# Performance work log

Hardware: AMD Instinct MI355X
Metric: run time of the kernel (lower is better)

## Reference

```python
import jax, jax.numpy as jnp
import numpy as np

N = 50000; E = 800000; F_IN = 128; H = 16; G = 256
DIMS = [F_IN, H, 2 * H, 4 * H, 4 * H, 8 * H]
EPS = 1e-5


def setup_inputs() -> dict:
    key = jax.random.key(0)
    ks = iter(jax.random.split(key, 40))
    inp = {}
    inp["x"] = jax.random.normal(next(ks), (N, F_IN), dtype=jnp.float32)
    inp["edge_index"] = jax.random.randint(next(ks), (2, E), 0, N, dtype=jnp.int32)
    inp["edge_weight"] = jax.random.uniform(next(ks), (E,), dtype=jnp.float32)
    inp["batch"] = jnp.sort(jax.random.randint(next(ks), (N,), 0, G, dtype=jnp.int32))
    for i in range(5):
        din, dout = DIMS[i], DIMS[i + 1]
        inp[f"W{i+1}"] = jax.random.normal(next(ks), (din, dout), dtype=jnp.float32) / np.sqrt(din).astype(np.float32)
        inp[f"b{i+1}"] = jnp.zeros((dout,), jnp.float32)
        inp[f"g{i+1}"] = jnp.ones((dout,), jnp.float32)
        inp[f"bt{i+1}"] = jnp.zeros((dout,), jnp.float32)
    inp["fc1_w"] = jax.random.normal(next(ks), (8 * H, 4 * H), dtype=jnp.float32) / np.sqrt(8 * H).astype(np.float32)
    inp["fc1_b"] = jnp.zeros((4 * H,), jnp.float32)
    inp["fc2_w"] = jax.random.normal(next(ks), (4 * H, 1), dtype=jnp.float32) / np.sqrt(4 * H).astype(np.float32)
    inp["fc2_b"] = jnp.zeros((1,), jnp.float32)
    return inp


def _gcn_norm(edge_index, edge_weight, n):
    # PyG GCNConv: add self-loops (weight 1), symmetric deg^-1/2 normalization.
    loop = jnp.arange(n, dtype=edge_index.dtype)
    row = jnp.concatenate([edge_index[0], loop])  # source
    col = jnp.concatenate([edge_index[1], loop])  # target
    w = jnp.concatenate([edge_weight, jnp.ones((n,), edge_weight.dtype)])
    deg = jax.ops.segment_sum(w, col, num_segments=n)
    dis = jnp.where(deg > 0, jax.lax.rsqrt(jnp.maximum(deg, 1e-12)), 0.0)
    return row, col, dis[row] * w * dis[col]


def _bn(h, g, b):
    # BatchNorm1d, training-mode batch statistics (biased variance, eps=1e-5)
    mu = h.mean(0)
    v = h.var(0)
    return g * (h - mu) * jax.lax.rsqrt(v + EPS) + b


def reference(x, edge_index, edge_weight, batch,
              W1, b1, g1, bt1, W2, b2, g2, bt2, W3, b3, g3, bt3,
              W4, b4, g4, bt4, W5, b5, g5, bt5,
              fc1_w, fc1_b, fc2_w, fc2_b):
    n = x.shape[0]
    row, col, norm = _gcn_norm(edge_index, edge_weight, n)

    def conv(h, W, b):
        m = h @ W                                   # [N, dout] dense transform
        agg = jax.ops.segment_sum(m[row] * norm[:, None], col, num_segments=n)
        return agg + b

    h = _bn(jax.nn.relu(conv(x, W1, b1)), g1, bt1)
    h = _bn(jax.nn.relu(conv(h, W2, b2)), g2, bt2)
    h = _bn(jax.nn.relu(conv(h, W3, b3)), g3, bt3)
    h = jax.nn.relu(_bn(conv(h, W4, b4), g4, bt4))   # layer4: conv->bn->relu
    h = _bn(conv(h, W5, b5), g5, bt5)                # layer5: conv->bn
    pooled = jax.ops.segment_sum(h, batch, num_segments=G)  # global_add_pool -> [G, 8H]
    p = jax.nn.relu(pooled)
    p = jax.nn.relu(p @ fc1_w + fc1_b)
    # dropout is identity in eval mode
    return (p @ fc2_w + fc2_b).reshape(-1)          # [G]
```

## Files before the change

### kernel.cpp

```cpp
#include <hip/hip_runtime.h>
#include <hip/hip_fp16.h>
#include <stdint.h>

#define NN 50000
#define NE 800000
#define NG 256
#define NBUCKET 16
#define PARTSZ (NBUCKET * 256)

#define NBKT 391
#define ABLK 391
#define ASLICE 2048
#define BCAP 2560

__device__ __forceinline__ float bf2f(unsigned short u) {
    return __uint_as_float(((unsigned)u) << 16);
}
__device__ __forceinline__ unsigned short f2bf(float f) {
    unsigned b = __float_as_uint(f);
    return (unsigned short)((b + 0x7FFF + ((b >> 16) & 1)) >> 16);
}
__device__ __forceinline__ unsigned short f2h(float f) {
    __half h = __float2half(f);
    return *(unsigned short*)&h;
}
__device__ __forceinline__ float h2f(unsigned short u) {
    __half h = *(__half*)&u;
    return __half2float(h);
}

#define AFF4(u, sc, sh) { u.x = fmaxf(sc.x*u.x+sh.x,0.f); u.y = fmaxf(sc.y*u.y+sh.y,0.f); \
                          u.z = fmaxf(sc.z*u.z+sh.z,0.f); u.w = fmaxf(sc.w*u.w+sh.w,0.f); }

__device__ __forceinline__ void scan_totals(const int* __restrict__ totals,
                                            int* __restrict__ sbase, int tid) {
    if (tid < 64) {
        const int C = (NBKT + 63) / 64;
        int tv[C];
        int s = 0;
        int i0 = tid * C;
#pragma unroll
        for (int j = 0; j < C; ++j) {
            int idx = i0 + j;
            int x = (idx < NBKT) ? totals[idx] : 0;
            tv[j] = x; s += x;
        }
        int inc = s;
        for (int off = 1; off < 64; off <<= 1) {
            int t2 = __shfl_up(inc, off, 64);
            if (tid >= off) inc += t2;
        }
        int run = inc - s;
#pragma unroll
        for (int j = 0; j < C; ++j) {
            int idx = i0 + j;
            if (idx < NBKT) sbase[idx] = run;
            run += tv[j];
        }
        if (tid == 63) sbase[NBKT] = run;
    }
}

__global__ void kA1(const int* __restrict__ col, int* __restrict__ bb, float* part, int e) {
    __shared__ int cnt[NBKT];
    for (int j = threadIdx.x; j < NBKT; j += 256) cnt[j] = 0;
    for (int i = blockIdx.x * 256 + threadIdx.x; i < 5 * PARTSZ; i += ABLK * 256) part[i] = 0.f;
    __syncthreads();
    int start = blockIdx.x * ASLICE;
    int end = min(start + ASLICE, e);
    for (int i = start + threadIdx.x; i < end; i += 256)
        atomicAdd(&cnt[col[i] >> 7], 1);
    __syncthreads();
    for (int j = threadIdx.x; j < NBKT; j += 256) bb[blockIdx.x * NBKT + j] = cnt[j];
}

__global__ void kA2a(int* __restrict__ bb, int* __restrict__ totals) {
    __shared__ int v[ABLK];
    int k = blockIdx.x;
    int tid = threadIdx.x;
    for (int b = tid; b < ABLK; b += 256) v[b] = bb[b * NBKT + k];
    __syncthreads();
    if (tid < 64) {
        const int C = (ABLK + 63) / 64;
        int tv[C];
        int s = 0;
        int i0 = tid * C;
#pragma unroll
        for (int j = 0; j < C; ++j) {
            int idx = i0 + j;
            int x = (idx < ABLK) ? v[idx] : 0;
            tv[j] = x; s += x;
        }
        int inc = s;
        for (int off = 1; off < 64; off <<= 1) {
            int t2 = __shfl_up(inc, off, 64);
            if (tid >= off) inc += t2;
        }
        int run = inc - s;
#pragma unroll
        for (int j = 0; j < C; ++j) {
            int idx = i0 + j;
            if (idx < ABLK) v[idx] = run;
            run += tv[j];
        }
        if (tid == 63) totals[k] = run;
    }
    __syncthreads();
    for (int b = tid; b < ABLK; b += 256) bb[b * NBKT + k] = v[b];
}

__global__ void kA3g(const int* __restrict__ row, const int* __restrict__ col,
                     const float* __restrict__ ew, const int* __restrict__ bb,
                     const int* __restrict__ totals, int2* __restrict__ staging,
                     const float* __restrict__ x, const float* __restrict__ W0,
                     float* __restrict__ m1, int e, int n) {
    __shared__ int cur[NBKT];
    __shared__ int sbase[NBKT + 1];
    __shared__ float Wl[128 * 16];
    int tid = threadIdx.x;
    if ((int)blockIdx.x < ABLK) {
        scan_totals(totals, sbase, tid);
        __syncthreads();
        for (int j = tid; j < NBKT; j += 256)
            cur[j] = sbase[j] + bb[blockIdx.x * NBKT + j];
        __syncthreads();
        int start = blockIdx.x * ASLICE;
        int end = min(start + ASLICE, e);
        for (int i = start + tid; i < end; i += 256) {
            int c = col[i];
            int p = atomicAdd(&cur[c >> 7], 1);
            staging[p] = make_int2(row[i] | ((c & 127) << 16), __float_as_int(ew[i]));
        }
        return;
    }
    int bid = (int)blockIdx.x - ABLK;
    for (int i = tid; i < 128 * 16 / 4; i += 256)
        ((float4*)Wl)[i] = ((const float4*)W0)[i];
    __syncthreads();
    int jq = tid % 4, group = tid / 4;
    int node0 = (bid * 64 + group) * 2;
    const float4* h4 = (const float4*)x;
    int hb[2]; bool val[2];
#pragma unroll
    for (int i = 0; i < 2; ++i) {
        int nd = node0 + i;
        val[i] = nd < n;
        hb[i] = (val[i] ? nd : n - 1) * 32;
    }
    float4 acc[2];
    acc[0] = {0,0,0,0}; acc[1] = {0,0,0,0};
#pragma unroll 4
    for (int k4 = 0; k4 < 32; ++k4) {
        const float* wb = &Wl[(k4 * 4) * 16 + jq * 4];
        float4 w0 = *(const float4*)(wb);
        float4 w1 = *(const float4*)(wb + 16);
        float4 w2 = *(const float4*)(wb + 32);
        float4 w3 = *(const float4*)(wb + 48);
#pragma unroll
        for (int i = 0; i < 2; ++i) {
            float4 hv = h4[hb[i] + k4];
            acc[i].x += hv.x*w0.x + hv.y*w1.x + hv.z*w2.x + hv.w*w3.x;
            acc[i].y += hv.x*w0.y + hv.y*w1.y + hv.z*w2.y + hv.w*w3.y;
            acc[i].z += hv.x*w0.z + hv.y*w1.z + hv.z*w2.z + hv.w*w3.z;
            acc[i].w += hv.x*w0.w + hv.y*w1.w + hv.z*w2.w + hv.w*w3.w;
        }
    }
#pragma unroll
    for (int i = 0; i < 2; ++i)
        if (val[i]) ((float4*)m1)[(node0 + i) * 4 + jq] = acc[i];
}

__global__ void __launch_bounds__(256) kB(const int* __restrict__ totals,
                                          const int2* __restrict__ staging,
                                          unsigned int* __restrict__ csr, int* __restrict__ ptr,
                                          float* __restrict__ dis, int n) {
    __shared__ int2 st[BCAP];
    __shared__ unsigned int outb[BCAP];
    __shared__ int hist[129];
    __shared__ int cur[128];
    __shared__ int sbase[NBKT + 1];
    int k = blockIdx.x, t = threadIdx.x;
    scan_totals(totals, sbase, t);
    if (t < 129) hist[t] = 0;
    __syncthreads();
    int base = sbase[k], cnt = sbase[k + 1] - sbase[k];
    int node0 = k << 7;
    int ncov = min(128, n - node0);
    if (cnt <= BCAP) {
        for (int i = t; i < cnt; i += 256) {
            int2 v = staging[base + i];
            st[i] = v;
            atomicAdd(&hist[v.x >> 16], 1);
        }
        __syncthreads();
        if (t == 0) {
            int run = 0;
            for (int j = 0; j < 128; ++j) { int h = hist[j]; hist[j] = run; run += h; }
            hist[128] = run;
        }
        __syncthreads();
        if (t < 128) cur[t] = hist[t];
        if (t < ncov) ptr[node0 + t] = base + hist[t];
        __syncthreads();
        for (int i = t; i < cnt; i += 256) {
            int2 v = st[i];
            int j = v.x >> 16;
            int p = atomicAdd(&cur[j], 1);
            outb[p] = (unsigned)(v.x & 0xFFFF) | ((unsigned)f2h(__int_as_float(v.y)) << 16);
        }
        __syncthreads();
        for (int i = t; i < cnt; i += 256) csr[base + i] = outb[i];
        if (t < ncov) {
            float s = 1.f;
            int a = hist[t], b2 = hist[t + 1];
            for (int p = a; p < b2; ++p) s += h2f((unsigned short)(outb[p] >> 16));
            dis[node0 + t] = rsqrtf(s);
        }
    } else {
        for (int i = t; i < cnt; i += 256) atomicAdd(&hist[staging[base + i].x >> 16], 1);
        __syncthreads();
        if (t == 0) {
            int run = 0;
            for (int j = 0; j < 128; ++j) { int h = hist[j]; hist[j] = run; run += h; }
            hist[128] = run;
        }
        __syncthreads();
        if (t < 128) cur[t] = hist[t];
        if (t < ncov) ptr[node0 + t] = base + hist[t];
        __syncthreads();
        for (int i = t; i < cnt; i += 256) {
            int2 v = staging[base + i];
            int j = v.x >> 16;
            int p = atomicAdd(&cur[j], 1);
            csr[base + p] = (unsigned)(v.x & 0xFFFF) | ((unsigned)f2h(__int_as_float(v.y)) << 16);
        }
        __threadfence_block();
        __syncthreads();
        if (t < ncov) {
            float s = 1.f;
            int a = hist[t], b2 = hist[t + 1];
            for (int p = a; p < b2; ++p) s += h2f((unsigned short)(csr[base + p] >> 16));
            dis[node0 + t] = rsqrtf(s);
        }
    }
    if (k == gridDim.x - 1 && t == 0) ptr[n] = sbase[NBKT];
}

__global__ void k_l1gather(const float* __restrict__ src, const int* __restrict__ ptr,
                           unsigned int* __restrict__ csr, const float* __restrict__ dis,
                           const float* __restrict__ bias, float* __restrict__ partOut,
                           float* __restrict__ out, int n) {
    __shared__ float ls[16], lq[16];
    int tid = threadIdx.x;
    if (tid < 16) { ls[tid] = 0.f; lq[tid] = 0.f; }
    __syncthreads();
    int t = blockIdx.x * 256 + tid;
    int node = t >> 2;
    int l4 = t & 3;
    bool valid = node < n;
    int nc = valid ? node : n - 1;
    const float4* s4 = (const float4*)src;
    float dc = dis[nc];
    float w0 = dc * dc;
    float4 v = s4[nc * 4 + l4];
    float4 acc = { w0 * v.x, w0 * v.y, w0 * v.z, w0 * v.w };
    int p0 = ptr[nc], p1 = ptr[nc + 1];
    int p = p0;
    for (; p + 4 <= p1; p += 4) {
        unsigned int c0 = csr[p], c1 = csr[p+1], c2 = csr[p+2], c3 = csr[p+3];
        int s0i = c0 & 0xFFFF, s1i = c1 & 0xFFFF, s2i = c2 & 0xFFFF, s3i = c3 & 0xFFFF;
        float e0 = dis[s0i] * h2f((unsigned short)(c0 >> 16)) * dc;
        float e1 = dis[s1i] * h2f((unsigned short)(c1 >> 16)) * dc;
        float e2 = dis[s2i] * h2f((unsigned short)(c2 >> 16)) * dc;
        float e3 = dis[s3i] * h2f((unsigned short)(c3 >> 16)) * dc;
        float4 u0 = s4[s0i * 4 + l4];
        float4 u1 = s4[s1i * 4 + l4];
        float4 u2 = s4[s2i * 4 + l4];
        float4 u3 = s4[s3i * 4 + l4];
        acc.x += e0*u0.x + e1*u1.x + e2*u2.x + e3*u3.x;
        acc.y += e0*u0.y + e1*u1.y + e2*u2.y + e3*u3.y;
        acc.z += e0*u0.z + e1*u1.z + e2*u2.z + e3*u3.z;
        acc.w += e0*u0.w + e1*u1.w + e2*u2.w + e3*u3.w;
        if (l4 == 0) {
            csr[p]   = (unsigned)s0i | ((unsigned)f2h(e0) << 16);
            csr[p+1] = (unsigned)s1i | ((unsigned)f2h(e1) << 16);
            csr[p+2] = (unsigned)s2i | ((unsigned)f2h(e2) << 16);
            csr[p+3] = (unsigned)s3i | ((unsigned)f2h(e3) << 16);
        }
    }
    for (; p < p1; ++p) {
        unsigned int ce = csr[p];
        int si = ce & 0xFFFF;
        float w = dis[si] * h2f((unsigned short)(ce >> 16)) * dc;
        float4 u = s4[si * 4 + l4];
        acc.x += w*u.x; acc.y += w*u.y; acc.z += w*u.z; acc.w += w*u.w;
        if (l4 == 0) csr[p] = (unsigned)si | ((unsigned)f2h(w) << 16);
    }
    float4 b = ((const float4*)bias)[l4];
    acc.x = fmaxf(acc.x + b.x, 0.f);
    acc.y = fmaxf(acc.y + b.y, 0.f);
    acc.z = fmaxf(acc.z + b.z, 0.f);
    acc.w = fmaxf(acc.w + b.w, 0.f);
    if (valid) ((float4*)out)[nc * 4 + l4] = acc;
    float s0 = valid ? acc.x : 0.f, s1 = valid ? acc.y : 0.f;
    float s2 = valid ? acc.z : 0.f, s3 = valid ? acc.w : 0.f;
    float q0 = s0*s0, q1 = s1*s1, q2 = s2*s2, q3 = s3*s3;
    for (int off = 4; off < 64; off <<= 1) {
        s0 += __shfl_down(s0, off, 64); s1 += __shfl_down(s1, off, 64);
        s2 += __shfl_down(s2, off, 64); s3 += __shfl_down(s3, off, 64);
        q0 += __shfl_down(q0, off, 64); q1 += __shfl_down(q1, off, 64);
        q2 += __shfl_down(q2, off, 64); q3 += __shfl_down(q3, off, 64);
    }
    int lane = tid & 63;
    if (lane < 4) {
        atomicAdd(&ls[4*lane+0], s0); atomicAdd(&ls[4*lane+1], s1);
        atomicAdd(&ls[4*lane+2], s2); atomicAdd(&ls[4*lane+3], s3);
        atomicAdd(&lq[4*lane+0], q0); atomicAdd(&lq[4*lane+1], q1);
        atomicAdd(&lq[4*lane+2], q2); atomicAdd(&lq[4*lane+3], q3);
    }
    __syncthreads();
    int bkt = (blockIdx.x & (NBUCKET - 1)) * 256;
    if (tid < 16) {
        atomicAdd(&partOut[bkt + tid], ls[tid]);
        atomicAdd(&partOut[bkt + 128 + tid], lq[tid]);
    }
}

template <int D, int BF16>
__device__ __forceinline__ float4 load_row(const void* src, int node, int l4) {
    if (BF16) {
        const unsigned short* sb = (const unsigned short*)src;
        ushort4 r = *(const ushort4*)(sb + (size_t)node * D + (l4 << 2));
        float4 f;
        f.x = bf2f(r.x); f.y = bf2f(r.y); f.z = bf2f(r.z); f.w = bf2f(r.w);
        return f;
    } else {
        const float4* s4 = (const float4*)src;
        return s4[(size_t)node * (D / 4) + l4];
    }
}

template <int D>
__device__ __forceinline__ void ldrow16(const unsigned short* __restrict__ src, int node, int l8,
                                        float4& a, float4& b) {
    uint4 r = *(const uint4*)(src + (size_t)node * D + (l8 << 3));
    a.x = bf2f((unsigned short)(r.x)); a.y = bf2f((unsigned short)(r.x >> 16));
    a.z = bf2f((unsigned short)(r.y)); a.w = bf2f((unsigned short)(r.y >> 16));
    b.x = bf2f((unsigned short)(r.z)); b.y = bf2f((unsigned short)(r.z >> 16));
    b.z = bf2f((unsigned short)(r.w)); b.w = bf2f((unsigned short)(r.w >> 16));
}

template <int DIN, int DOUT, int EP, int POSTAFF, int PREAFF, int RELU,
          int BF16IN, int BF16OUT, int NPB>
__global__ void __launch_bounds__(256) k_fused(
        const void* __restrict__ src, const int* __restrict__ ptr,
        const unsigned int* __restrict__ csr, const float* __restrict__ dis,
        const float* __restrict__ partIn, const float* __restrict__ gmv,
        const float* __restrict__ btv, const float* __restrict__ W,
        const float* __restrict__ bias, float* __restrict__ partOut,
        void* __restrict__ out, int n) {
    const int TPN1 = DIN / 4, LPN = TPN1 * EP, GN1 = 256 / LPN;
    const int TPN2 = DOUT / 4, G2 = 256 / TPN2;
    const int HS = DIN + 4;
    __shared__ float Wl[DIN * DOUT];
    __shared__ float hrow[NPB * HS];
    __shared__ float scs[DIN], shs[DIN];
    __shared__ float ls[DOUT], lq[DOUT];
    int tid = threadIdx.x;
    for (int i = tid; i < DIN * DOUT / 4; i += 256)
        ((float4*)Wl)[i] = ((const float4*)W)[i];
    if (tid < DIN) {
        float s = 0.f, q = 0.f;
#pragma unroll
        for (int b2 = 0; b2 < NBUCKET; ++b2) {
            s += partIn[b2 * 256 + tid];
            q += partIn[b2 * 256 + 128 + tid];
        }
        float mu = s / (float)n;
        float var = q / (float)n - mu * mu;
        float a = gmv[tid] * rsqrtf(var + 1e-5f);
        scs[tid] = a;
        shs[tid] = btv[tid] - mu * a;
    }
    if (tid < DOUT) { ls[tid] = 0.f; lq[tid] = 0.f; }
    __syncthreads();

    int nodebase = blockIdx.x * NPB;
    {
        int grp = tid / LPN, r = tid % LPN;
        int e0 = r / TPN1, l4 = r % TPN1;
        float4 sc = ((const float4*)scs)[l4];
        float4 sh = ((const float4*)shs)[l4];
#pragma unroll
        for (int pass = 0; pass < NPB / GN1; ++pass) {
            int nl = pass * GN1 + grp;
            int node = nodebase + nl;
            int nc = node < n ? node : n - 1;
            float4 acc = {0.f, 0.f, 0.f, 0.f};
            float sumw = 0.f;
            if (e0 == 0) {
                float d = dis[nc];
                float w0 = d * d;
                float4 v = load_row<DIN, BF16IN>(src, nc, l4);
                if (PREAFF) AFF4(v, sc, sh);
                acc.x = w0*v.x; acc.y = w0*v.y; acc.z = w0*v.z; acc.w = w0*v.w;
                sumw = w0;
            }
            int p0 = ptr[nc], p1 = ptr[nc + 1];
            int p = p0 + e0;
            for (; p + 3 * EP < p1; p += 4 * EP) {
                unsigned int c0 = csr[p], c1 = csr[p + EP], c2 = csr[p + 2*EP], c3 = csr[p + 3*EP];
                float e0w = h2f((unsigned short)(c0 >> 16)), e1w = h2f((unsigned short)(c1 >> 16));
                float e2w = h2f((unsigned short)(c2 >> 16)), e3w = h2f((unsigned short)(c3 >> 16));
                float4 u0 = load_row<DIN, BF16IN>(src, c0 & 0xFFFF, l4);
                float4 u1 = load_row<DIN, BF16IN>(src, c1 & 0xFFFF, l4);
                float4 u2 = load_row<DIN, BF16IN>(src, c2 & 0xFFFF, l4);
                float4 u3 = load_row<DIN, BF16IN>(src, c3 & 0xFFFF, l4);
                if (PREAFF) { AFF4(u0, sc, sh); AFF4(u1, sc, sh); AFF4(u2, sc, sh); AFF4(u3, sc, sh); }
                acc.x += e0w*u0.x + e1w*u1.x + e2w*u2.x + e3w*u3.x;
                acc.y += e0w*u0.y + e1w*u1.y + e2w*u2.y + e3w*u3.y;
                acc.z += e0w*u0.z + e1w*u1.z + e2w*u2.z + e3w*u3.z;
                acc.w += e0w*u0.w + e1w*u1.w + e2w*u2.w + e3w*u3.w;
                if (POSTAFF) sumw += e0w + e1w + e2w + e3w;
            }
            for (; p < p1; p += EP) {
                unsigned int ce = csr[p];
                float w = h2f((unsigned short)(ce >> 16));
                float4 u = load_row<DIN, BF16IN>(src, ce & 0xFFFF, l4);
                if (PREAFF) AFF4(u, sc, sh);
                acc.x += w*u.x; acc.y += w*u.y; acc.z += w*u.z; acc.w += w*u.w;
                if (POSTAFF) sumw += w;
            }
#pragma unroll
            for (int off = TPN1; off < LPN; off <<= 1) {
                acc.x += __shfl_xor(acc.x, off, 64);
                acc.y += __shfl_xor(acc.y, off, 64);
                acc.z += __shfl_xor(acc.z, off, 64);
                acc.w += __shfl_xor(acc.w, off, 64);
                if (POSTAFF) sumw += __shfl_xor(sumw, off, 64);
            }
            if (POSTAFF) {
                acc.x = sc.x * acc.x + sh.x * sumw;
                acc.y = sc.y * acc.y + sh.y * sumw;
                acc.z = sc.z * acc.z + sh.z * sumw;
                acc.w = sc.w * acc.w + sh.w * sumw;
            }
            if (e0 == 0) *(float4*)&hrow[nl * HS + (l4 << 2)] = acc;
        }
    }
    __syncthreads();
    {
        int jq = tid % TPN2, g2 = tid / TPN2;
        float4 bv = ((const float4*)bias)[jq];
        float4 sv = {0,0,0,0}, qv = {0,0,0,0};
        for (int nl = g2; nl < NPB; nl += G2) {
            int node = nodebase + nl;
            bool valid = node < n;
            float4 a = {0.f, 0.f, 0.f, 0.f};
#pragma unroll
            for (int k4 = 0; k4 < DIN / 4; ++k4) {
                float4 hv = *(const float4*)&hrow[nl * HS + (k4 << 2)];
                const float* wb = &Wl[(k4 * 4) * DOUT + jq * 4];
                float4 w0 = *(const float4*)(wb);
                float4 w1 = *(const float4*)(wb + DOUT);
                float4 w2 = *(const float4*)(wb + 2 * DOUT);
                float4 w3 = *(const float4*)(wb + 3 * DOUT);
                a.x += hv.x*w0.x + hv.y*w1.x + hv.z*w2.x + hv.w*w3.x;
                a.y += hv.x*w0.y + hv.y*w1.y + hv.z*w2.y + hv.w*w3.y;
                a.z += hv.x*w0.z + hv.y*w1.z + hv.z*w2.z + hv.w*w3.z;
                a.w += hv.x*w0.w + hv.y*w1.w + hv.z*w2.w + hv.w*w3.w;
            }
            a.x += bv.x; a.y += bv.y; a.z += bv.z; a.w += bv.w;
            if (RELU) {
                a.x = fmaxf(a.x, 0.f); a.y = fmaxf(a.y, 0.f);
                a.z = fmaxf(a.z, 0.f); a.w = fmaxf(a.w, 0.f);
            }
            if (valid) {
                if (BF16OUT) {
                    ushort4 o;
                    o.x = f2bf(a.x); o.y = f2bf(a.y); o.z = f2bf(a.z); o.w = f2bf(a.w);
                    *(ushort4*)((unsigned short*)out + (size_t)node * DOUT + (jq << 2)) = o;
                } else {
                    ((float4*)out)[(size_t)node * TPN2 + jq] = a;
                }
                sv.x += a.x; sv.y += a.y; sv.z += a.z; sv.w += a.w;
                qv.x += a.x*a.x; qv.y += a.y*a.y; qv.z += a.z*a.z; qv.w += a.w*a.w;
            }
        }
        for (int off = TPN2; off < 64; off <<= 1) {
            sv.x += __shfl_down(sv.x, off, 64); sv.y += __shfl_down(sv.y, off, 64);
            sv.z += __shfl_down(sv.z, off, 64); sv.w += __shfl_down(sv.w, off, 64);
            qv.x += __shfl_down(qv.x, off, 64); qv.y += __shfl_down(qv.y, off, 64);
            qv.z += __shfl_down(qv.z, off, 64); qv.w += __shfl_down(qv.w, off, 64);
        }
        int lane = tid & 63;
        if (lane < TPN2) {
            atomicAdd(&ls[4*lane+0], sv.x); atomicAdd(&ls[4*lane+1], sv.y);
            atomicAdd(&ls[4*lane+2], sv.z); atomicAdd(&ls[4*lane+3], sv.w);
            atomicAdd(&lq[4*lane+0], qv.x); atomicAdd(&lq[4*lane+1], qv.y);
            atomicAdd(&lq[4*lane+2], qv.z); atomicAdd(&lq[4*lane+3], qv.w);
        }
        __syncthreads();
        int bkt = (blockIdx.x & (NBUCKET - 1)) * 256;
        if (tid < DOUT) {
            atomicAdd(&partOut[bkt + tid], ls[tid]);
            atomicAdd(&partOut[bkt + 128 + tid], lq[tid]);
        }
    }
}

template <int D, int POSTAFF, int PREAFF>
__global__ void __launch_bounds__(256) k_wgather(
        const unsigned short* __restrict__ src, const int* __restrict__ ptr,
        const unsigned int* __restrict__ csr, const float* __restrict__ dis,
        const float* __restrict__ partIn, const float* __restrict__ gmv,
        const float* __restrict__ btv, float* __restrict__ out, int n) {
    const int RL = D / 8;
    const int EP = 4;
    const int LPN = RL * EP;
    __shared__ float scs[D], shs[D];
    int tid = threadIdx.x;
    if (tid < D) {
        float s = 0.f, q = 0.f;
#pragma unroll
        for (int b2 = 0; b2 < NBUCKET; ++b2) {
            s += partIn[b2 * 256 + tid];
            q += partIn[b2 * 256 + 128 + tid];
        }
        float mu = s / (float)n;
        float var = q / (float)n - mu * mu;
        float a = gmv[tid] * rsqrtf(var + 1e-5f);
        scs[tid] = a;
        shs[tid] = btv[tid] - mu * a;
    }
    __syncthreads();
    int t = blockIdx.x * 256 + tid;
    int node = t / LPN;
    int r = t - node * LPN;
    int e0 = r / RL;
    int l8 = r - e0 * RL;
    bool valid = node < n;
    int nc = valid ? node : n - 1;
    float4 scA = ((const float4*)scs)[l8 * 2],     shA = ((const float4*)shs)[l8 * 2];
    float4 scB = ((const float4*)scs)[l8 * 2 + 1], shB = ((const float4*)shs)[l8 * 2 + 1];
    float4 accA = {0.f,0.f,0.f,0.f}, accB = {0.f,0.f,0.f,0.f};
    float sumw = 0.f;
    if (e0 == 0) {
        float d = dis[nc];
        float w0 = d * d;
        float4 a, b2;
        ldrow16<D>(src, nc, l8, a, b2);
        if (PREAFF) { AFF4(a, scA, shA); AFF4(b2, scB, shB); }
        accA.x = w0*a.x;  accA.y = w0*a.y;  accA.z = w0*a.z;  accA.w = w0*a.w;
        accB.x = w0*b2.x; accB.y = w0*b2.y; accB.z = w0*b2.z; accB.w = w0*b2.w;
        sumw = w0;
    }
    int p0 = ptr[nc], p1 = ptr[nc + 1];
    int p = p0 + e0;
    for (; p + 3 * EP < p1; p += 4 * EP) {
        unsigned int c0 = csr[p], c1 = csr[p + EP], c2 = csr[p + 2*EP], c3 = csr[p + 3*EP];
        float w0 = h2f((unsigned short)(c0 >> 16)), w1 = h2f((unsigned short)(c1 >> 16));
        float w2 = h2f((unsigned short)(c2 >> 16)), w3 = h2f((unsigned short)(c3 >> 16));
        float4 a0, b0, a1, b1, a2, b2, a3, b3;
        ldrow16<D>(src, c0 & 0xFFFF, l8, a0, b0);
        ldrow16<D>(src, c1 & 0xFFFF, l8, a1, b1);
        ldrow16<D>(src, c2 & 0xFFFF, l8, a2, b2);
        ldrow16<D>(src, c3 & 0xFFFF, l8, a3, b3);
        if (PREAFF) {
            AFF4(a0, scA, shA); AFF4(b0, scB, shB);
            AFF4(a1, scA, shA); AFF4(b1, scB, shB);
            AFF4(a2, scA, shA); AFF4(b2, scB, shB);
            AFF4(a3, scA, shA); AFF4(b3, scB, shB);
        }
        accA.x += w0*a0.x + w1*a1.x + w2*a2.x + w3*a3.x;
        accA.y += w0*a0.y + w1*a1.y + w2*a2.y + w3*a3.y;
        accA.z += w0*a0.z + w1*a1.z + w2*a2.z + w3*a3.z;
        accA.w += w0*a0.w + w1*a1.w + w2*a2.w + w3*a3.w;
        accB.x += w0*b0.x + w1*b1.x + w2*b2.x + w3*b3.x;
        accB.y += w0*b0.y + w1*b1.y + w2*b2.y + w3*b3.y;
        accB.z += w0*b0.z + w1*b1.z + w2*b2.z + w3*b3.z;
        accB.w += w0*b0.w + w1*b1.w + w2*b2.w + w3*b3.w;
        if (POSTAFF) sumw += w0 + w1 + w2 + w3;
    }
    for (; p < p1; p += EP) {
        unsigned int ce = csr[p];
        float w = h2f((unsigned short)(ce >> 16));
        float4 a, b2;
        ldrow16<D>(src, ce & 0xFFFF, l8, a, b2);
        if (PREAFF) { AFF4(a, scA, shA); AFF4(b2, scB, shB); }
        accA.x += w*a.x;  accA.y += w*a.y;  accA.z += w*a.z;  accA.w += w*a.w;
        accB.x += w*b2.x; accB.y += w*b2.y; accB.z += w*b2.z; accB.w += w*b2.w;
        if (POSTAFF) sumw += w;
    }
#pragma unroll
    for (int off = RL; off < LPN; off <<= 1) {
        accA.x += __shfl_xor(accA.x, off, 64); accA.y += __shfl_xor(accA.y, off, 64);
        accA.z += __shfl_xor(accA.z, off, 64); accA.w += __shfl_xor(accA.w, off, 64);
        accB.x += __shfl_xor(accB.x, off, 64); accB.y += __shfl_xor(accB.y, off, 64);
        accB.z += __shfl_xor(accB.z, off, 64); accB.w += __shfl_xor(accB.w, off, 64);
        if (POSTAFF) sumw += __shfl_xor(sumw, off, 64);
    }
    if (POSTAFF) {
        accA.x = scA.x * accA.x + shA.x * sumw; accA.y = scA.y * accA.y + shA.y * sumw;
        accA.z = scA.z * accA.z + shA.z * sumw; accA.w = scA.w * accA.w + shA.w * sumw;
        accB.x = scB.x * accB.x + shB.x * sumw; accB.y = scB.y * accB.y + shB.y * sumw;
        accB.z = scB.z * accB.z + shB.z * sumw; accB.w = scB.w * accB.w + shB.w * sumw;
    }
    if (valid && e0 == 0) {
        ((float4*)out)[(size_t)nc * (D / 4) + l8 * 2]     = accA;
        ((float4*)out)[(size_t)nc * (D / 4) + l8 * 2 + 1] = accB;
    }
}

template <int DIN, int DOUT, int RELU, int BF16OUT>
__global__ void k_sgemm(const float* __restrict__ h, const float* __restrict__ W,
                        const float* __restrict__ bias, float* __restrict__ partOut,
                        void* __restrict__ m, int n) {
    const int TPN = DOUT / 4, GPB = 256 / TPN, NPT = 4;
    __shared__ float Wl[DIN * DOUT];
    __shared__ float ls[DOUT], lq[DOUT];
    int tid = threadIdx.x;
    for (int i = tid; i < DIN * DOUT / 4; i += 256)
        ((float4*)Wl)[i] = ((const float4*)W)[i];
    if (tid < DOUT) { ls[tid] = 0.f; lq[tid] = 0.f; }
    __syncthreads();

    int jq = tid % TPN;
    int group = tid / TPN;
    int node0 = (blockIdx.x * GPB + group) * NPT;
    const float4* h4 = (const float4*)h;
    int hb[NPT]; bool val[NPT];
#pragma unroll
    for (int i = 0; i < NPT; ++i) {
        int nd = node0 + i;
        val[i] = nd < n;
        hb[i] = (val[i] ? nd : n - 1) * (DIN / 4);
    }
    float4 acc[NPT];
#pragma unroll
    for (int i = 0; i < NPT; ++i) acc[i] = {0.f, 0.f, 0.f, 0.f};
#pragma unroll 4
    for (int k4 = 0; k4 < DIN / 4; ++k4) {
        const float* wb = &Wl[(k4 * 4) * DOUT + jq * 4];
        float4 w0 = *(const float4*)(wb);
        float4 w1 = *(const float4*)(wb + DOUT);
        float4 w2 = *(const float4*)(wb + 2 * DOUT);
        float4 w3 = *(const float4*)(wb + 3 * DOUT);
#pragma unroll
        for (int i = 0; i < NPT; ++i) {
            float4 hv = h4[hb[i] + k4];
            acc[i].x += hv.x*w0.x + hv.y*w1.x + hv.z*w2.x + hv.w*w3.x;
            acc[i].y += hv.x*w0.y + hv.y*w1.y + hv.z*w2.y + hv.w*w3.y;
            acc[i].z += hv.x*w0.z + hv.y*w1.z + hv.z*w2.z + hv.w*w3.z;
            acc[i].w += hv.x*w0.w + hv.y*w1.w + hv.z*w2.w + hv.w*w3.w;
        }
    }
    float4 bv = ((const float4*)bias)[jq];
    float4 sv = {0,0,0,0}, qv = {0,0,0,0};
#pragma unroll
    for (int i = 0; i < NPT; ++i) {
        float4 a = acc[i];
        a.x += bv.x; a.y += bv.y; a.z += bv.z; a.w += bv.w;
        if (RELU) {
            a.x = fmaxf(a.x, 0.f); a.y = fmaxf(a.y, 0.f);
            a.z = fmaxf(a.z, 0.f); a.w = fmaxf(a.w, 0.f);
        }
        if (val[i]) {
            if (BF16OUT) {
                ushort4 o;
                o.x = f2bf(a.x); o.y = f2bf(a.y); o.z = f2bf(a.z); o.w = f2bf(a.w);
                *(ushort4*)((unsigned short*)m + (size_t)(node0 + i) * DOUT + (jq << 2)) = o;
            } else {
                ((float4*)m)[(size_t)(node0 + i) * TPN + jq] = a;
            }
            sv.x += a.x; sv.y += a.y; sv.z += a.z; sv.w += a.w;
            qv.x += a.x*a.x; qv.y += a.y*a.y; qv.z += a.z*a.z; qv.w += a.w*a.w;
        }
    }
    for (int off = TPN; off < 64; off <<= 1) {
        sv.x += __shfl_down(sv.x, off, 64); sv.y += __shfl_down(sv.y, off, 64);
        sv.z += __shfl_down(sv.z, off, 64); sv.w += __shfl_down(sv.w, off, 64);
        qv.x += __shfl_down(qv.x, off, 64); qv.y += __shfl_down(qv.y, off, 64);
        qv.z += __shfl_down(qv.z, off, 64); qv.w += __shfl_down(qv.w, off, 64);
    }
    int lane = tid & 63;
    if (lane < TPN) {
        atomicAdd(&ls[4*lane+0], sv.x); atomicAdd(&ls[4*lane+1], sv.y);
        atomicAdd(&ls[4*lane+2], sv.z); atomicAdd(&ls[4*lane+3], sv.w);
        atomicAdd(&lq[4*lane+0], qv.x); atomicAdd(&lq[4*lane+1], qv.y);
        atomicAdd(&lq[4*lane+2], qv.z); atomicAdd(&lq[4*lane+3], qv.w);
    }
    __syncthreads();
    int bkt = (blockIdx.x & (NBUCKET - 1)) * 256;
    if (tid < DOUT) {
        atomicAdd(&partOut[bkt + tid], ls[tid]);
        atomicAdd(&partOut[bkt + 128 + tid], lq[tid]);
    }
}

__global__ void k_poolhead(const float* __restrict__ h, const int* __restrict__ batch,
                           const float* __restrict__ partIn, const float* __restrict__ gmv,
                           const float* __restrict__ btv,
                           const float* __restrict__ fc1w, const float* __restrict__ fc1b,
                           const float* __restrict__ fc2w, const float* __restrict__ fc2b,
                           float* __restrict__ out, int n) {
    __shared__ float tmp[256];
    __shared__ float pl[128];
    __shared__ float scs[128], shs[128];
    int g = blockIdx.x;
    int tid = threadIdx.x;
    if (tid < 128) {
        float s = 0.f, q = 0.f;
#pragma unroll
        for (int b2 = 0; b2 < NBUCKET; ++b2) {
            s += partIn[b2 * 256 + tid];
            q += partIn[b2 * 256 + 128 + tid];
        }
        float mu = s / (float)n;
        float var = q / (float)n - mu * mu;
        float a = gmv[tid] * rsqrtf(var + 1e-5f);
        scs[tid] = a;
        shs[tid] = btv[tid] - mu * a;
    }
    int j = tid & 127, prt = tid >> 7;
    int a = 0, b = n;
    while (a < b) { int mid = (a + b) >> 1; if (batch[mid] < g) a = mid + 1; else b = mid; }
    int lo = a;
    b = n;
    while (a < b) { int mid = (a + b) >> 1; if (batch[mid] < g + 1) a = mid + 1; else b = mid; }
    int hi = a;

    float acc = 0.f;
    for (int node = lo + prt; node < hi; node += 2) acc += h[(long)node * 128 + j];
    tmp[tid] = acc;
    __syncthreads();
    if (tid < 128) {
        float cnt = (float)(hi - lo);
        float p = scs[tid] * (tmp[tid] + tmp[tid + 128]) + shs[tid] * cnt;
        pl[tid] = fmaxf(p, 0.f);
    }
    __syncthreads();
    if (tid < 64) {
        float v1 = fc1b[tid];
        for (int k = 0; k < 128; ++k) v1 += pl[k] * fc1w[k * 64 + tid];
        v1 = fmaxf(v1, 0.f);
        float v = v1 * fc2w[tid];
        for (int off = 32; off > 0; off >>= 1) v += __shfl_down(v, off, 64);
        if (tid == 0) out[g] = v + fc2b[0];
    }
}

extern "C" void kernel_launch(void* const* d_in, const int* in_sizes, int n_in,
                              void* d_out, int out_size, void* d_ws, size_t ws_size,
                              hipStream_t stream) {
    const float* x     = (const float*)d_in[0];
    const int*   ei    = (const int*)d_in[1];
    const float* ew    = (const float*)d_in[2];
    const int*   batch = (const int*)d_in[3];
    const float *W[5], *b[5], *gm[5], *bt[5];
    for (int i = 0; i < 5; ++i) {
        W[i]  = (const float*)d_in[4 + 4 * i];
        b[i]  = (const float*)d_in[5 + 4 * i];
        gm[i] = (const float*)d_in[6 + 4 * i];
        bt[i] = (const float*)d_in[7 + 4 * i];
    }
    const float* fc1w = (const float*)d_in[24];
    const float* fc1b = (const float*)d_in[25];
    const float* fc2w = (const float*)d_in[26];
    const float* fc2b = (const float*)d_in[27];
    float* out = (float*)d_out;

    char* wsb = (char*)d_ws;
    float* dis    = (float*)wsb;  wsb += sizeof(float) * NN;
    int*   ptr    = (int*)wsb;    wsb += sizeof(int) * (NN + 4);
    int*   bb     = (int*)wsb;    wsb += sizeof(int) * ABLK * NBKT;
    int*   totals = (int*)wsb;    wsb += sizeof(int) * (NBKT + 1);
    wsb = (char*)(((uintptr_t)wsb + 15) & ~(uintptr_t)15);
    int2*  staging= (int2*)wsb;   wsb += sizeof(int2) * NE;
    unsigned int* csru = (unsigned int*)wsb; wsb += sizeof(unsigned int) * NE;
    wsb = (char*)(((uintptr_t)wsb + 15) & ~(uintptr_t)15);
    float* part   = (float*)wsb;  wsb += sizeof(float) * 5 * PARTSZ;
    unsigned short* bufB1 = (unsigned short*)wsb;  wsb += sizeof(unsigned short) * (size_t)NN * 64;
    unsigned short* bufB2 = (unsigned short*)wsb;  wsb += sizeof(unsigned short) * (size_t)NN * 64;
    float* buf1   = (float*)wsb;  wsb += sizeof(float) * (size_t)NN * 64;
    float* buf2   = (float*)wsb;  wsb += sizeof(float) * (size_t)NN * 128;

    const int* row = ei;
    const int* col = ei + NE;
    const int B = 256;
    const int NBF = (NN + 15) / 16;
    const int GB1 = (NN + 127) / 128;

    kA1<<<ABLK, B, 0, stream>>>(col, bb, part, NE);
    kA2a<<<NBKT, B, 0, stream>>>(bb, totals);
    kA3g<<<ABLK + GB1, B, 0, stream>>>(row, col, ew, bb, totals, staging, x, W[0], buf1, NE, NN);
    kB<<<NBKT, B, 0, stream>>>(totals, staging, csru, ptr, dis, NN);

    k_l1gather<<<(NN * 4 + 255) / 256, B, 0, stream>>>(buf1, ptr, csru, dis,
                                                       b[0], part + 0 * PARTSZ, buf2, NN);

    k_fused<16, 32, 4, 1, 0, 1, 0, 1, 16><<<NBF, B, 0, stream>>>(
        buf2, ptr, csru, dis, part + 0 * PARTSZ, gm[0], bt[0],
        W[1], b[1], part + 1 * PARTSZ, bufB1, NN);

    k_wgather<32, 1, 0><<<(int)(((long)NN * 16 + 255) / 256), B, 0, stream>>>(
        bufB1, ptr, csru, dis, part + 1 * PARTSZ, gm[1], bt[1], buf1, NN);
    k_sgemm<32, 64, 1, 1><<<(NN + 63) / 64, B, 0, stream>>>(buf1, W[2], b[2], part + 2 * PARTSZ, bufB2, NN);

    k_wgather<64, 1, 0><<<(int)(((long)NN * 32 + 255) / 256), B, 0, stream>>>(
        bufB2, ptr, csru, dis, part + 2 * PARTSZ, gm[2], bt[2], buf1, NN);
    k_sgemm<64, 64, 0, 1><<<(NN + 63) / 64, B, 0, stream>>>(buf1, W[3], b[3], part + 3 * PARTSZ, bufB1, NN);

    k_wgather<64, 0, 1><<<(int)(((long)NN * 32 + 255) / 256), B, 0, stream>>>(
        bufB1, ptr, csru, dis, part + 3 * PARTSZ, gm[3], bt[3], buf1, NN);
    k_sgemm<64, 128, 0, 0><<<(NN + 31) / 32, B, 0, stream>>>(buf1, W[4], b[4], part + 4 * PARTSZ, buf2, NN);

    k_poolhead<<<NG, B, 0, stream>>>(buf2, batch, part + 4 * PARTSZ, gm[4], bt[4],
                                     fc1w, fc1b, fc2w, fc2b, out, NN);
}
```

Measured before the change: 361.7 us.

## Switch to fp32/fp64 accumulation and fuse global pooling into final GEMM

Replaces the half-precision packed CSR and bf16 intermediate buffers with int2 CSR entries carrying fp32 weights and fp32 activations. Gather accumulators and batch-norm statistics move to double precision, with double atomics. Global add pooling is fused into the last sgemm through per-block shared double accumulators, and the 128-wide layer-5 output buffer is no longer written. The main aim looks like accuracy. Memory traffic roughly doubles and fp64 arithmetic and atomics are added, partly offset by skipping the layer-5 write and re-read.

```diff
diff --git a/kernel.cpp b/kernel.cpp
--- a/kernel.cpp
+++ b/kernel.cpp
@@ -1,5 +1,4 @@
 #include <hip/hip_runtime.h>
-#include <hip/hip_fp16.h>
 #include <stdint.h>
 
 #define NN 50000
@@ -13,24 +12,25 @@
 #define ASLICE 2048
 #define BCAP 2560
 
-__device__ __forceinline__ float bf2f(unsigned short u) {
-    return __uint_as_float(((unsigned)u) << 16);
-}
-__device__ __forceinline__ unsigned short f2bf(float f) {
-    unsigned b = __float_as_uint(f);
-    return (unsigned short)((b + 0x7FFF + ((b >> 16) & 1)) >> 16);
-}
-__device__ __forceinline__ unsigned short f2h(float f) {
-    __half h = __float2half(f);
-    return *(unsigned short*)&h;
-}
-__device__ __forceinline__ float h2f(unsigned short u) {
-    __half h = *(__half*)&u;
-    return __half2float(h);
-}
-
 #define AFF4(u, sc, sh) { u.x = fmaxf(sc.x*u.x+sh.x,0.f); u.y = fmaxf(sc.y*u.y+sh.y,0.f); \
                           u.z = fmaxf(sc.z*u.z+sh.z,0.f); u.w = fmaxf(sc.w*u.w+sh.w,0.f); }
+
+__device__ __forceinline__ void bn_coef(const double* __restrict__ partIn,
+                                        const float* __restrict__ gmv,
+                                        const float* __restrict__ btv,
+                                        int tid, int n, float* scs, float* shs) {
+    double s = 0., q = 0.;
+#pragma unroll
+    for (int b2 = 0; b2 < NBUCKET; ++b2) {
+        s += partIn[b2 * 256 + tid];
+        q += partIn[b2 * 256 + 128 + tid];
+    }
+    double mu = s / (double)n;
+    double var = q / (double)n - mu * mu;
+    float a = gmv[tid] * rsqrtf((float)var + 1e-5f);
+    scs[tid] = a;
+    shs[tid] = btv[tid] - (float)mu * a;
+}
 
 __device__ __forceinline__ void scan_totals(const int* __restrict__ totals,
                                             int* __restrict__ sbase, int tid) {
@@ -61,10 +61,11 @@
     }
 }
 
-__global__ void kA1(const int* __restrict__ col, int* __restrict__ bb, float* part, int e) {
+__global__ void kA1(const int* __restrict__ col, int* __restrict__ bb,
+                    double* __restrict__ zz, int zn, int e) {
     __shared__ int cnt[NBKT];
     for (int j = threadIdx.x; j < NBKT; j += 256) cnt[j] = 0;
-    for (int i = blockIdx.x * 256 + threadIdx.x; i < 5 * PARTSZ; i += ABLK * 256) part[i] = 0.f;
+    for (int i = blockIdx.x * 256 + threadIdx.x; i < zn; i += ABLK * 256) zz[i] = 0.;
     __syncthreads();
     int start = blockIdx.x * ASLICE;
     int end = min(start + ASLICE, e);
@@ -172,10 +173,10 @@
 
 __global__ void __launch_bounds__(256) kB(const int* __restrict__ totals,
                                           const int2* __restrict__ staging,
-                                          unsigned int* __restrict__ csr, int* __restrict__ ptr,
+                                          int2* __restrict__ csr, int* __restrict__ ptr,
                                           float* __restrict__ dis, int n) {
     __shared__ int2 st[BCAP];
-    __shared__ unsigned int outb[BCAP];
+    __shared__ int2 outb[BCAP];
     __shared__ int hist[129];
     __shared__ int cur[128];
     __shared__ int sbase[NBKT + 1];
@@ -206,15 +207,15 @@
             int2 v = st[i];
             int j = v.x >> 16;
             int p = atomicAdd(&cur[j], 1);
-            outb[p] = (unsigned)(v.x & 0xFFFF) | ((unsigned)f2h(__int_as_float(v.y)) << 16);
+            outb[p] = make_int2(v.x & 0xFFFF, v.y);
         }
         __syncthreads();
         for (int i = t; i < cnt; i += 256) csr[base + i] = outb[i];
         if (t < ncov) {
-            float s = 1.f;
+            double s = 1.;
             int a = hist[t], b2 = hist[t + 1];
-            for (int p = a; p < b2; ++p) s += h2f((unsigned short)(outb[p] >> 16));
-            dis[node0 + t] = rsqrtf(s);
+            for (int p = a; p < b2; ++p) s += (double)__int_as_float(outb[p].y);
+            dis[node0 + t] = rsqrtf((float)s);
         }
     } else {
         for (int i = t; i < cnt; i += 256) atomicAdd(&hist[staging[base + i].x >> 16], 1);
@@ -232,28 +233,25 @@
             int2 v = staging[base + i];
             int j = v.x >> 16;
             int p = atomicAdd(&cur[j], 1);
-            csr[base + p] = (unsigned)(v.x & 0xFFFF) | ((unsigned)f2h(__int_as_float(v.y)) << 16);
+            csr[base + p] = make_int2(v.x & 0xFFFF, v.y);
         }
         __threadfence_block();
         __syncthreads();
         if (t < ncov) {
-            float s = 1.f;
+            double s = 1.;
             int a = hist[t], b2 = hist[t + 1];
-            for (int p = a; p < b2; ++p) s += h2f((unsigned short)(csr[base + p] >> 16));
-            dis[node0 + t] = rsqrtf(s);
+            for (int p = a; p < b2; ++p) s += (double)__int_as_float(csr[base + p].y);
+            dis[node0 + t] = rsqrtf((float)s);
         }
     }
     if (k == gridDim.x - 1 && t == 0) ptr[n] = sbase[NBKT];
 }
 
 __global__ void k_l1gather(const float* __restrict__ src, const int* __restrict__ ptr,
-                           unsigned int* __restrict__ csr, const float* __restrict__ dis,
-                           const float* __restrict__ bias, float* __restrict__ partOut,
+                           int2* __restrict__ csr, const float* __restrict__ dis,
+                           const float* __restrict__ bias, double* __restrict__ partOut,
                            float* __restrict__ out, int n) {
-    __shared__ float ls[16], lq[16];
     int tid = threadIdx.x;
-    if (tid < 16) { ls[tid] = 0.f; lq[tid] = 0.f; }
-    __syncthreads();
     int t = blockIdx.x * 256 + tid;
     int node = t >> 2;
     int l4 = t & 3;
@@ -263,44 +261,45 @@
     float dc = dis[nc];
     float w0 = dc * dc;
     float4 v = s4[nc * 4 + l4];
-    float4 acc = { w0 * v.x, w0 * v.y, w0 * v.z, w0 * v.w };
+    double ax = (double)(w0 * v.x), ay = (double)(w0 * v.y);
+    double az = (double)(w0 * v.z), aw = (double)(w0 * v.w);
     int p0 = ptr[nc], p1 = ptr[nc + 1];
     int p = p0;
     for (; p + 4 <= p1; p += 4) {
-        unsigned int c0 = csr[p], c1 = csr[p+1], c2 = csr[p+2], c3 = csr[p+3];
-        int s0i = c0 & 0xFFFF, s1i = c1 & 0xFFFF, s2i = c2 & 0xFFFF, s3i = c3 & 0xFFFF;
-        float e0 = dis[s0i] * h2f((unsigned short)(c0 >> 16)) * dc;
-        float e1 = dis[s1i] * h2f((unsigned short)(c1 >> 16)) * dc;
-        float e2 = dis[s2i] * h2f((unsigned short)(c2 >> 16)) * dc;
-        float e3 = dis[s3i] * h2f((unsigned short)(c3 >> 16)) * dc;
-        float4 u0 = s4[s0i * 4 + l4];
-        float4 u1 = s4[s1i * 4 + l4];
-        float4 u2 = s4[s2i * 4 + l4];
-        float4 u3 = s4[s3i * 4 + l4];
-        acc.x += e0*u0.x + e1*u1.x + e2*u2.x + e3*u3.x;
-        acc.y += e0*u0.y + e1*u1.y + e2*u2.y + e3*u3.y;
-        acc.z += e0*u0.z + e1*u1.z + e2*u2.z + e3*u3.z;
-        acc.w += e0*u0.w + e1*u1.w + e2*u2.w + e3*u3.w;
+        int2 c0 = csr[p], c1 = csr[p+1], c2 = csr[p+2], c3 = csr[p+3];
+        float e0 = dis[c0.x] * __int_as_float(c0.y) * dc;
+        float e1 = dis[c1.x] * __int_as_float(c1.y) * dc;
+        float e2 = dis[c2.x] * __int_as_float(c2.y) * dc;
+        float e3 = dis[c3.x] * __int_as_float(c3.y) * dc;
+        float4 u0 = s4[c0.x * 4 + l4];
+        float4 u1 = s4[c1.x * 4 + l4];
+        float4 u2 = s4[c2.x * 4 + l4];
+        float4 u3 = s4[c3.x * 4 + l4];
+        ax += (double)(e0*u0.x) + (double)(e1*u1.x) + (double)(e2*u2.x) + (double)(e3*u3.x);
+        ay += (double)(e0*u0.y) + (double)(e1*u1.y) + (double)(e2*u2.y) + (double)(e3*u3.y);
+        az += (double)(e0*u0.z) + (double)(e1*u1.z) + (double)(e2*u2.z) + (double)(e3*u3.z);
+        aw += (double)(e0*u0.w) + (double)(e1*u1.w) + (double)(e2*u2.w) + (double)(e3*u3.w);
         if (l4 == 0) {
-            csr[p]   = (unsigned)s0i | ((unsigned)f2h(e0) << 16);
-            csr[p+1] = (unsigned)s1i | ((unsigned)f2h(e1) << 16);
-            csr[p+2] = (unsigned)s2i | ((unsigned)f2h(e2) << 16);
-            csr[p+3] = (unsigned)s3i | ((unsigned)f2h(e3) << 16);
+            csr[p]   = make_int2(c0.x, __float_as_int(e0));
+            csr[p+1] = make_int2(c1.x, __float_as_int(e1));
+            csr[p+2] = make_int2(c2.x, __float_as_int(e2));
+            csr[p+3] = make_int2(c3.x, __float_as_int(e3));
         }
     }
     for (; p < p1; ++p) {
-        unsigned int ce = csr[p];
-        int si = ce & 0xFFFF;
-        float w = dis[si] * h2f((unsigned short)(ce >> 16)) * dc;
-        float4 u = s4[si * 4 + l4];
-        acc.x += w*u.x; acc.y += w*u.y; acc.z += w*u.z; acc.w += w*u.w;
-        if (l4 == 0) csr[p] = (unsigned)si | ((unsigned)f2h(w) << 16);
+        int2 ce = csr[p];
+        float w = dis[ce.x] * __int_as_float(ce.y) * dc;
+        float4 u = s4[ce.x * 4 + l4];
+        ax += (double)(w*u.x); ay += (double)(w*u.y);
+        az += (double)(w*u.z); aw += (double)(w*u.w);
+        if (l4 == 0) csr[p] = make_int2(ce.x, __float_as_int(w));
     }
     float4 b = ((const float4*)bias)[l4];
-    acc.x = fmaxf(acc.x + b.x, 0.f);
-    acc.y = fmaxf(acc.y + b.y, 0.f);
-    acc.z = fmaxf(acc.z + b.z, 0.f);
-    acc.w = fmaxf(acc.w + b.w, 0.f);
+    float4 acc;
+    acc.x = fmaxf((float)ax + b.x, 0.f);
+    acc.y = fmaxf((float)ay + b.y, 0.f);
+    acc.z = fmaxf((float)az + b.z, 0.f);
+    acc.w = fmaxf((float)aw + b.w, 0.f);
     if (valid) ((float4*)out)[nc * 4 + l4] = acc;
     float s0 = valid ? acc.x : 0.f, s1 = valid ? acc.y : 0.f;
     float s2 = valid ? acc.z : 0.f, s3 = valid ? acc.w : 0.f;
@@ -312,77 +311,39 @@
         q2 += __shfl_down(q2, off, 64); q3 += __shfl_down(q3, off, 64);
     }
     int lane = tid & 63;
+    int bkt = (blockIdx.x & (NBUCKET - 1)) * 256;
     if (lane < 4) {
-        atomicAdd(&ls[4*lane+0], s0); atomicAdd(&ls[4*lane+1], s1);
-        atomicAdd(&ls[4*lane+2], s2); atomicAdd(&ls[4*lane+3], s3);
-        atomicAdd(&lq[4*lane+0], q0); atomicAdd(&lq[4*lane+1], q1);
-        atomicAdd(&lq[4*lane+2], q2); atomicAdd(&lq[4*lane+3], q3);
-    }
-    __syncthreads();
-    int bkt = (blockIdx.x & (NBUCKET - 1)) * 256;
-    if (tid < 16) {
-        atomicAdd(&partOut[bkt + tid], ls[tid]);
-        atomicAdd(&partOut[bkt + 128 + tid], lq[tid]);
-    }
-}
-
-template <int D, int BF16>
-__device__ __forceinline__ float4 load_row(const void* src, int node, int l4) {
-    if (BF16) {
-        const unsigned short* sb = (const unsigned short*)src;
-        ushort4 r = *(const ushort4*)(sb + (size_t)node * D + (l4 << 2));
-        float4 f;
-        f.x = bf2f(r.x); f.y = bf2f(r.y); f.z = bf2f(r.z); f.w = bf2f(r.w);
-        return f;
-    } else {
-        const float4* s4 = (const float4*)src;
-        return s4[(size_t)node * (D / 4) + l4];
-    }
-}
-
-template <int D>
-__device__ __forceinline__ void ldrow16(const unsigned short* __restrict__ src, int node, int l8,
-                                        float4& a, float4& b) {
-    uint4 r = *(const uint4*)(src + (size_t)node * D + (l8 << 3));
-    a.x = bf2f((unsigned short)(r.x)); a.y = bf2f((unsigned short)(r.x >> 16));
-    a.z = bf2f((unsigned short)(r.y)); a.w = bf2f((unsigned short)(r.y >> 16));
-    b.x = bf2f((unsigned short)(r.z)); b.y = bf2f((unsigned short)(r.z >> 16));
-    b.z = bf2f((unsigned short)(r.w)); b.w = bf2f((unsigned short)(r.w >> 16));
-}
-
-template <int DIN, int DOUT, int EP, int POSTAFF, int PREAFF, int RELU,
-          int BF16IN, int BF16OUT, int NPB>
+        atomicAdd(&partOut[bkt + 4*lane + 0], (double)s0);
+        atomicAdd(&partOut[bkt + 4*lane + 1], (double)s1);
+        atomicAdd(&partOut[bkt + 4*lane + 2], (double)s2);
+        atomicAdd(&partOut[bkt + 4*lane + 3], (double)s3);
+        atomicAdd(&partOut[bkt + 128 + 4*lane + 0], (double)q0);
+        atomicAdd(&partOut[bkt + 128 + 4*lane + 1], (double)q1);
+        atomicAdd(&partOut[bkt + 128 + 4*lane + 2], (double)q2);
+        atomicAdd(&partOut[bkt + 128 + 4*lane + 3], (double)q3);
+    }
+}
+
+template <int DIN, int DOUT, int EP, int POSTAFF, int RELU, int NPB>
 __global__ void __launch_bounds__(256) k_fused(
-        const void* __restrict__ src, const int* __restrict__ ptr,
-        const unsigned int* __restrict__ csr, const float* __restrict__ dis,
-        const float* __restrict__ partIn, const float* __restrict__ gmv,
+        const float* __restrict__ src, const int* __restrict__ ptr,
+        const int2* __restrict__ csr, const float* __restrict__ dis,
+        const double* __restrict__ partIn, const float* __restrict__ gmv,
         const float* __restrict__ btv, const float* __restrict__ W,
-        const float* __restrict__ bias, float* __restrict__ partOut,
-        void* __restrict__ out, int n) {
+        const float* __restrict__ bias, double* __restrict__ partOut,
+        float* __restrict__ out, int n) {
     const int TPN1 = DIN / 4, LPN = TPN1 * EP, GN1 = 256 / LPN;
     const int TPN2 = DOUT / 4, G2 = 256 / TPN2;
     const int HS = DIN + 4;
     __shared__ float Wl[DIN * DOUT];
     __shared__ float hrow[NPB * HS];
     __shared__ float scs[DIN], shs[DIN];
-    __shared__ float ls[DOUT], lq[DOUT];
+    __shared__ double ls[DOUT], lq[DOUT];
     int tid = threadIdx.x;
     for (int i = tid; i < DIN * DOUT / 4; i += 256)
         ((float4*)Wl)[i] = ((const float4*)W)[i];
-    if (tid < DIN) {
-        float s = 0.f, q = 0.f;
-#pragma unroll
-        for (int b2 = 0; b2 < NBUCKET; ++b2) {
-            s += partIn[b2 * 256 + tid];
-            q += partIn[b2 * 256 + 128 + tid];
-        }
-        float mu = s / (float)n;
-        float var = q / (float)n - mu * mu;
-        float a = gmv[tid] * rsqrtf(var + 1e-5f);
-        scs[tid] = a;
-        shs[tid] = btv[tid] - mu * a;
-    }
-    if (tid < DOUT) { ls[tid] = 0.f; lq[tid] = 0.f; }
+    if (tid < DIN) bn_coef(partIn, gmv, btv, tid, n, scs, shs);
+    if (tid < DOUT) { ls[tid] = 0.; lq[tid] = 0.; }
     __syncthreads();
 
     int nodebase = blockIdx.x * NPB;
@@ -391,61 +352,63 @@
         int e0 = r / TPN1, l4 = r % TPN1;
         float4 sc = ((const float4*)scs)[l4];
         float4 sh = ((const float4*)shs)[l4];
+        const float4* s4 = (const float4*)src;
 #pragma unroll
         for (int pass = 0; pass < NPB / GN1; ++pass) {
             int nl = pass * GN1 + grp;
             int node = nodebase + nl;
             int nc = node < n ? node : n - 1;
-            float4 acc = {0.f, 0.f, 0.f, 0.f};
-            float sumw = 0.f;
+            double ax = 0., ay = 0., az = 0., aw = 0.;
+            double sumw = 0.;
             if (e0 == 0) {
                 float d = dis[nc];
                 float w0 = d * d;
-                float4 v = load_row<DIN, BF16IN>(src, nc, l4);
-                if (PREAFF) AFF4(v, sc, sh);
-                acc.x = w0*v.x; acc.y = w0*v.y; acc.z = w0*v.z; acc.w = w0*v.w;
-                sumw = w0;
+                float4 v = s4[(size_t)nc * TPN1 + l4];
+                ax = (double)(w0*v.x); ay = (double)(w0*v.y);
+                az = (double)(w0*v.z); aw = (double)(w0*v.w);
+                sumw = (double)w0;
             }
             int p0 = ptr[nc], p1 = ptr[nc + 1];
             int p = p0 + e0;
             for (; p + 3 * EP < p1; p += 4 * EP) {
-                unsigned int c0 = csr[p], c1 = csr[p + EP], c2 = csr[p + 2*EP], c3 = csr[p + 3*EP];
-                float e0w = h2f((unsigned short)(c0 >> 16)), e1w = h2f((unsigned short)(c1 >> 16));
-                float e2w = h2f((unsigned short)(c2 >> 16)), e3w = h2f((unsigned short)(c3 >> 16));
-                float4 u0 = load_row<DIN, BF16IN>(src, c0 & 0xFFFF, l4);
-                float4 u1 = load_row<DIN, BF16IN>(src, c1 & 0xFFFF, l4);
-                float4 u2 = load_row<DIN, BF16IN>(src, c2 & 0xFFFF, l4);
-                float4 u3 = load_row<DIN, BF16IN>(src, c3 & 0xFFFF, l4);
-                if (PREAFF) { AFF4(u0, sc, sh); AFF4(u1, sc, sh); AFF4(u2, sc, sh); AFF4(u3, sc, sh); }
-                acc.x += e0w*u0.x + e1w*u1.x + e2w*u2.x + e3w*u3.x;
-                acc.y += e0w*u0.y + e1w*u1.y + e2w*u2.y + e3w*u3.y;
-                acc.z += e0w*u0.z + e1w*u1.z + e2w*u2.z + e3w*u3.z;
-                acc.w += e0w*u0.w + e1w*u1.w + e2w*u2.w + e3w*u3.w;
-                if (POSTAFF) sumw += e0w + e1w + e2w + e3w;
+                int2 c0 = csr[p], c1 = csr[p + EP], c2 = csr[p + 2*EP], c3 = csr[p + 3*EP];
+                float e0w = __int_as_float(c0.y), e1w = __int_as_float(c1.y);
+                float e2w = __int_as_float(c2.y), e3w = __int_as_float(c3.y);
+                float4 u0 = s4[(size_t)c0.x * TPN1 + l4];
+                float4 u1 = s4[(size_t)c1.x * TPN1 + l4];
+                float4 u2 = s4[(size_t)c2.x * TPN1 + l4];
+                float4 u3 = s4[(size_t)c3.x * TPN1 + l4];
+                ax += (double)(e0w*u0.x) + (double)(e1w*u1.x) + (double)(e2w*u2.x) + (double)(e3w*u3.x);
+                ay += (double)(e0w*u0.y) + (double)(e1w*u1.y) + (double)(e2w*u2.y) + (double)(e3w*u3.y);
+                az += (double)(e0w*u0.z) + (double)(e1w*u1.z) + (double)(e2w*u2.z) + (double)(e3w*u3.z);
+                aw += (double)(e0w*u0.w) + (double)(e1w*u1.w) + (double)(e2w*u2.w) + (double)(e3w*u3.w);
+                if (POSTAFF) sumw += (double)e0w + (double)e1w + (double)e2w + (double)e3w;
             }
             for (; p < p1; p += EP) {
-                unsigned int ce = csr[p];
-                float w = h2f((unsigned short)(ce >> 16));
-                float4 u = load_row<DIN, BF16IN>(src, ce & 0xFFFF, l4);
-                if (PREAFF) AFF4(u, sc, sh);
-                acc.x += w*u.x; acc.y += w*u.y; acc.z += w*u.z; acc.w += w*u.w;
-                if (POSTAFF) sumw += w;
+                int2 ce = csr[p];
+                float w = __int_as_float(ce.y);
+                float4 u = s4[(size_t)ce.x * TPN1 + l4];
+                ax += (double)(w*u.x); ay += (double)(w*u.y);
+                az += (double)(w*u.z); aw += (double)(w*u.w);
+                if (POSTAFF) sumw += (double)w;
             }
 #pragma unroll
             for (int off = TPN1; off < LPN; off <<= 1) {
-                acc.x += __shfl_xor(acc.x, off, 64);
-                acc.y += __shfl_xor(acc.y, off, 64);
-                acc.z += __shfl_xor(acc.z, off, 64);
-                acc.w += __shfl_xor(acc.w, off, 64);
+                ax += __shfl_xor(ax, off, 64);
+                ay += __shfl_xor(ay, off, 64);
+                az += __shfl_xor(az, off, 64);
+                aw += __shfl_xor(aw, off, 64);
                 if (POSTAFF) sumw += __shfl_xor(sumw, off, 64);
             }
-            if (POSTAFF) {
-                acc.x = sc.x * acc.x + sh.x * sumw;
-                acc.y = sc.y * acc.y + sh.y * sumw;
-                acc.z = sc.z * acc.z + sh.z * sumw;
-                acc.w = sc.w * acc.w + sh.w * sumw;
-            }
-            if (e0 == 0) *(float4*)&hrow[nl * HS + (l4 << 2)] = acc;
+            if (e0 == 0) {
+                float4 acc;
+                float sw = (float)sumw;
+                acc.x = sc.x * (float)ax + sh.x * sw;
+                acc.y = sc.y * (float)ay + sh.y * sw;
+                acc.z = sc.z * (float)az + sh.z * sw;
+                acc.w = sc.w * (float)aw + sh.w * sw;
+                *(float4*)&hrow[nl * HS + (l4 << 2)] = acc;
+            }
         }
     }
     __syncthreads();
@@ -476,13 +439,7 @@
                 a.z = fmaxf(a.z, 0.f); a.w = fmaxf(a.w, 0.f);
             }
             if (valid) {
-                if (BF16OUT) {
-                    ushort4 o;
-                    o.x = f2bf(a.x); o.y = f2bf(a.y); o.z = f2bf(a.z); o.w = f2bf(a.w);
-                    *(ushort4*)((unsigned short*)out + (size_t)node * DOUT + (jq << 2)) = o;
-                } else {
-                    ((float4*)out)[(size_t)node * TPN2 + jq] = a;
-                }
+                ((float4*)out)[(size_t)node * TPN2 + jq] = a;
                 sv.x += a.x; sv.y += a.y; sv.z += a.z; sv.w += a.w;
                 qv.x += a.x*a.x; qv.y += a.y*a.y; qv.z += a.z*a.z; qv.w += a.w*a.w;
             }
@@ -495,10 +452,10 @@
         }
         int lane = tid & 63;
         if (lane < TPN2) {
-            atomicAdd(&ls[4*lane+0], sv.x); atomicAdd(&ls[4*lane+1], sv.y);
-            atomicAdd(&ls[4*lane+2], sv.z); atomicAdd(&ls[4*lane+3], sv.w);
-            atomicAdd(&lq[4*lane+0], qv.x); atomicAdd(&lq[4*lane+1], qv.y);
-            atomicAdd(&lq[4*lane+2], qv.z); atomicAdd(&lq[4*lane+3], qv.w);
+            atomicAdd(&ls[4*lane+0], (double)sv.x); atomicAdd(&ls[4*lane+1], (double)sv.y);
+            atomicAdd(&ls[4*lane+2], (double)sv.z); atomicAdd(&ls[4*lane+3], (double)sv.w);
+            atomicAdd(&lq[4*lane+0], (double)qv.x); atomicAdd(&lq[4*lane+1], (double)qv.y);
+            atomicAdd(&lq[4*lane+2], (double)qv.z); atomicAdd(&lq[4*lane+3], (double)qv.w);
         }
         __syncthreads();
         int bkt = (blockIdx.x & (NBUCKET - 1)) * 256;
@@ -511,118 +468,108 @@
 
 template <int D, int POSTAFF, int PREAFF>
 __global__ void __launch_bounds__(256) k_wgather(
-        const unsigned short* __restrict__ src, const int* __restrict__ ptr,
-        const unsigned int* __restrict__ csr, const float* __restrict__ dis,
-        const float* __restrict__ partIn, const float* __restrict__ gmv,
+        const float* __restrict__ src, const int* __restrict__ ptr,
+        const int2* __restrict__ csr, const float* __restrict__ dis,
+        const double* __restrict__ partIn, const float* __restrict__ gmv,
         const float* __restrict__ btv, float* __restrict__ out, int n) {
-    const int RL = D / 8;
+    const int RL = D / 4;
     const int EP = 4;
     const int LPN = RL * EP;
     __shared__ float scs[D], shs[D];
     int tid = threadIdx.x;
-    if (tid < D) {
-        float s = 0.f, q = 0.f;
-#pragma unroll
-        for (int b2 = 0; b2 < NBUCKET; ++b2) {
-            s += partIn[b2 * 256 + tid];
-            q += partIn[b2 * 256 + 128 + tid];
-        }
-        float mu = s / (float)n;
-        float var = q / (float)n - mu * mu;
-        float a = gmv[tid] * rsqrtf(var + 1e-5f);
-        scs[tid] = a;
-        shs[tid] = btv[tid] - mu * a;
-    }
+    if (tid < D) bn_coef(partIn, gmv, btv, tid, n, scs, shs);
     __syncthreads();
     int t = blockIdx.x * 256 + tid;
     int node = t / LPN;
     int r = t - node * LPN;
     int e0 = r / RL;
-    int l8 = r - e0 * RL;
+    int l4 = r - e0 * RL;
     bool valid = node < n;
     int nc = valid ? node : n - 1;
-    float4 scA = ((const float4*)scs)[l8 * 2],     shA = ((const float4*)shs)[l8 * 2];
-    float4 scB = ((const float4*)scs)[l8 * 2 + 1], shB = ((const float4*)shs)[l8 * 2 + 1];
-    float4 accA = {0.f,0.f,0.f,0.f}, accB = {0.f,0.f,0.f,0.f};
-    float sumw = 0.f;
+    const float4* s4 = (const float4*)src;
+    float4 sc = ((const float4*)scs)[l4], sh = ((const float4*)shs)[l4];
+    double ax = 0., ay = 0., az = 0., aw = 0.;
+    double sumw = 0.;
     if (e0 == 0) {
         float d = dis[nc];
         float w0 = d * d;
-        float4 a, b2;
-        ldrow16<D>(src, nc, l8, a, b2);
-        if (PREAFF) { AFF4(a, scA, shA); AFF4(b2, scB, shB); }
-        accA.x = w0*a.x;  accA.y = w0*a.y;  accA.z = w0*a.z;  accA.w = w0*a.w;
-        accB.x = w0*b2.x; accB.y = w0*b2.y; accB.z = w0*b2.z; accB.w = w0*b2.w;
-        sumw = w0;
+        float4 v = s4[(size_t)nc * RL + l4];
+        if (PREAFF) AFF4(v, sc, sh);
+        ax = (double)(w0*v.x); ay = (double)(w0*v.y);
+        az = (double)(w0*v.z); aw = (double)(w0*v.w);
+        sumw = (double)w0;
     }
     int p0 = ptr[nc], p1 = ptr[nc + 1];
     int p = p0 + e0;
     for (; p + 3 * EP < p1; p += 4 * EP) {
-        unsigned int c0 = csr[p], c1 = csr[p + EP], c2 = csr[p + 2*EP], c3 = csr[p + 3*EP];
-        float w0 = h2f((unsigned short)(c0 >> 16)), w1 = h2f((unsigned short)(c1 >> 16));
-        float w2 = h2f((unsigned short)(c2 >> 16)), w3 = h2f((unsigned short)(c3 >> 16));
-        float4 a0, b0, a1, b1, a2, b2, a3, b3;
-        ldrow16<D>(src, c0 & 0xFFFF, l8, a0, b0);
-        ldrow16<D>(src, c1 & 0xFFFF, l8, a1, b1);
-        ldrow16<D>(src, c2 & 0xFFFF, l8, a2, b2);
-        ldrow16<D>(src, c3 & 0xFFFF, l8, a3, b3);
-        if (PREAFF) {
-            AFF4(a0, scA, shA); AFF4(b0, scB, shB);
-            AFF4(a1, scA, shA); AFF4(b1, scB, shB);
-            AFF4(a2, scA, shA); AFF4(b2, scB, shB);
-            AFF4(a3, scA, shA); AFF4(b3, scB, shB);
-        }
-        accA.x += w0*a0.x + w1*a1.x + w2*a2.x + w3*a3.x;
-        accA.y += w0*a0.y + w1*a1.y + w2*a2.y + w3*a3.y;
-        accA.z += w0*a0.z + w1*a1.z + w2*a2.z + w3*a3.z;
-        accA.w += w0*a0.w + w1*a1.w + w2*a2.w + w3*a3.w;
-        accB.x += w0*b0.x + w1*b1.x + w2*b2.x + w3*b3.x;
-        accB.y += w0*b0.y + w1*b1.y + w2*b2.y + w3*b3.y;
-        accB.z += w0*b0.z + w1*b1.z + w2*b2.z + w3*b3.z;
-        accB.w += w0*b0.w + w1*b1.w + w2*b2.w + w3*b3.w;
-        if (POSTAFF) sumw += w0 + w1 + w2 + w3;
+        int2 c0 = csr[p], c1 = csr[p + EP], c2 = csr[p + 2*EP], c3 = csr[p + 3*EP];
+        float w0 = __int_as_float(c0.y), w1 = __int_as_float(c1.y);
+        float w2 = __int_as_float(c2.y), w3 = __int_as_float(c3.y);
+        float4 u0 = s4[(size_t)c0.x * RL + l4];
+        float4 u1 = s4[(size_t)c1.x * RL + l4];
+        float4 u2 = s4[(size_t)c2.x * RL + l4];
+        float4 u3 = s4[(size_t)c3.x * RL + l4];
+        if (PREAFF) { AFF4(u0, sc, sh); AFF4(u1, sc, sh); AFF4(u2, sc, sh); AFF4(u3, sc, sh); }
+        ax += (double)(w0*u0.x) + (double)(w1*u1.x) + (double)(w2*u2.x) + (double)(w3*u3.x);
+        ay += (double)(w0*u0.y) + (double)(w1*u1.y) + (double)(w2*u2.y) + (double)(w3*u3.y);
+        az += (double)(w0*u0.z) + (double)(w1*u1.z) + (double)(w2*u2.z) + (double)(w3*u3.z);
+        aw += (double)(w0*u0.w) + (double)(w1*u1.w) + (double)(w2*u2.w) + (double)(w3*u3.w);
+        if (POSTAFF) sumw += (double)w0 + (double)w1 + (double)w2 + (double)w3;
     }
     for (; p < p1; p += EP) {
-        unsigned int ce = csr[p];
-        float w = h2f((unsigned short)(ce >> 16));
-        float4 a, b2;
-        ldrow16<D>(src, ce & 0xFFFF, l8, a, b2);
-        if (PREAFF) { AFF4(a, scA, shA); AFF4(b2, scB, shB); }
-        accA.x += w*a.x;  accA.y += w*a.y;  accA.z += w*a.z;  accA.w += w*a.w;
-        accB.x += w*b2.x; accB.y += w*b2.y; accB.z += w*b2.z; accB.w += w*b2.w;
-        if (POSTAFF) sumw += w;
+        int2 ce = csr[p];
+        float w = __int_as_float(ce.y);
+        float4 u = s4[(size_t)ce.x * RL + l4];
+        if (PREAFF) AFF4(u, sc, sh);
+        ax += (double)(w*u.x); ay += (double)(w*u.y);
+        az += (double)(w*u.z); aw += (double)(w*u.w);
+        if (POSTAFF) sumw += (double)w;
     }
 #pragma unroll
     for (int off = RL; off < LPN; off <<= 1) {
-        accA.x += __shfl_xor(accA.x, off, 64); accA.y += __shfl_xor(accA.y, off, 64);
-        accA.z += __shfl_xor(accA.z, off, 64); accA.w += __shfl_xor(accA.w, off, 64);
-        accB.x += __shfl_xor(accB.x, off, 64); accB.y += __shfl_xor(accB.y, off, 64);
-        accB.z += __shfl_xor(accB.z, off, 64); accB.w += __shfl_xor(accB.w, off, 64);
+        ax += __shfl_xor(ax, off, 64); ay += __shfl_xor(ay, off, 64);
+        az += __shfl_xor(az, off, 64); aw += __shfl_xor(aw, off, 64);
         if (POSTAFF) sumw += __shfl_xor(sumw, off, 64);
     }
-    if (POSTAFF) {
-        accA.x = scA.x * accA.x + shA.x * sumw; accA.y = scA.y * accA.y + shA.y * sumw;
-        accA.z = scA.z * accA.z + shA.z * sumw; accA.w = scA.w * accA.w + shA.w * sumw;
-        accB.x = scB.x * accB.x + shB.x * sumw; accB.y = scB.y * accB.y + shB.y * sumw;
-        accB.z = scB.z * accB.z + shB.z * sumw; accB.w = scB.w * accB.w + shB.w * sumw;
-    }
     if (valid && e0 == 0) {
-        ((float4*)out)[(size_t)nc * (D / 4) + l8 * 2]     = accA;
-        ((float4*)out)[(size_t)nc * (D / 4) + l8 * 2 + 1] = accB;
-    }
-}
-
-template <int DIN, int DOUT, int RELU, int BF16OUT>
+        float4 acc;
+        if (POSTAFF) {
+            float sw = (float)sumw;
+            acc.x = sc.x * (float)ax + sh.x * sw;
+            acc.y = sc.y * (float)ay + sh.y * sw;
+            acc.z = sc.z * (float)az + sh.z * sw;
+            acc.w = sc.w * (float)aw + sh.w * sw;
+        } else {
+            acc.x = (float)ax; acc.y = (float)ay;
+            acc.z = (float)az; acc.w = (float)aw;
+        }
+        ((float4*)out)[(size_t)nc * RL + l4] = acc;
+    }
+}
+
+template <int DIN, int DOUT, int RELU, int POOL>
 __global__ void k_sgemm(const float* __restrict__ h, const float* __restrict__ W,
-                        const float* __restrict__ bias, float* __restrict__ partOut,
-                        void* __restrict__ m, int n) {
+                        const float* __restrict__ bias, double* __restrict__ partOut,
+                        float* __restrict__ m, const int* __restrict__ batch,
+                        double* __restrict__ pooled, int n) {
     const int TPN = DOUT / 4, GPB = 256 / TPN, NPT = 4;
+    const int NPBLK = GPB * NPT;
+    const int MAXG = 34;
     __shared__ float Wl[DIN * DOUT];
-    __shared__ float ls[DOUT], lq[DOUT];
+    __shared__ double ls[DOUT], lq[DOUT];
+    __shared__ double pool_l[POOL ? MAXG * DOUT : 1];
+    __shared__ int gmaxs;
     int tid = threadIdx.x;
     for (int i = tid; i < DIN * DOUT / 4; i += 256)
         ((float4*)Wl)[i] = ((const float4*)W)[i];
-    if (tid < DOUT) { ls[tid] = 0.f; lq[tid] = 0.f; }
+    if (tid < DOUT) { ls[tid] = 0.; lq[tid] = 0.; }
+    int gbase = 0;
+    if (POOL) {
+        for (int i = tid; i < MAXG * DOUT; i += 256) pool_l[i] = 0.;
+        if (tid == 0) gmaxs = 0;
+        int bn0 = blockIdx.x * NPBLK;
+        gbase = batch[bn0 < n ? bn0 : n - 1];
+    }
     __syncthreads();
 
     int jq = tid % TPN;
@@ -666,10 +613,19 @@
             a.z = fmaxf(a.z, 0.f); a.w = fmaxf(a.w, 0.f);
         }
         if (val[i]) {
-            if (BF16OUT) {
-                ushort4 o;
-                o.x = f2bf(a.x); o.y = f2bf(a.y); o.z = f2bf(a.z); o.w = f2bf(a.w);
-                *(ushort4*)((unsigned short*)m + (size_t)(node0 + i) * DOUT + (jq << 2)) = o;
+            if (POOL) {
+                int off = batch[node0 + i] - gbase;
+                if (off < MAXG) {
+                    atomicAdd(&pool_l[off * DOUT + jq * 4 + 0], (double)a.x);
+                    atomicAdd(&pool_l[off * DOUT + jq * 4 + 1], (double)a.y);
+                    atomicAdd(&pool_l[off * DOUT + jq * 4 + 2], (double)a.z);
+                    atomicAdd(&pool_l[off * DOUT + jq * 4 + 3], (double)a.w);
+                    if (jq == 0) atomicMax(&gmaxs, off);
+                } else {
+                    double* pg = &pooled[(size_t)(gbase + off) * DOUT + jq * 4];
+                    atomicAdd(pg + 0, (double)a.x); atomicAdd(pg + 1, (double)a.y);
+                    atomicAdd(pg + 2, (double)a.z); atomicAdd(pg + 3, (double)a.w);
+                }
             } else {
                 ((float4*)m)[(size_t)(node0 + i) * TPN + jq] = a;
             }
@@ -685,10 +641,10 @@
     }
     int lane = tid & 63;
     if (lane < TPN) {
-        atomicAdd(&ls[4*lane+0], sv.x); atomicAdd(&ls[4*lane+1], sv.y);
-        atomicAdd(&ls[4*lane+2], sv.z); atomicAdd(&ls[4*lane+3], sv.w);
-        atomicAdd(&lq[4*lane+0], qv.x); atomicAdd(&lq[4*lane+1], qv.y);
-        atomicAdd(&lq[4*lane+2], qv.z); atomicAdd(&lq[4*lane+3], qv.w);
+        atomicAdd(&ls[4*lane+0], (double)sv.x); atomicAdd(&ls[4*lane+1], (double)sv.y);
+        atomicAdd(&ls[4*lane+2], (double)sv.z); atomicAdd(&ls[4*lane+3], (double)sv.w);
+        atomicAdd(&lq[4*lane+0], (double)qv.x); atomicAdd(&lq[4*lane+1], (double)qv.y);
+        atomicAdd(&lq[4*lane+2], (double)qv.z); atomicAdd(&lq[4*lane+3], (double)qv.w);
     }
     __syncthreads();
     int bkt = (blockIdx.x & (NBUCKET - 1)) * 256;
@@ -696,49 +652,36 @@
         atomicAdd(&partOut[bkt + tid], ls[tid]);
         atomicAdd(&partOut[bkt + 128 + tid], lq[tid]);
     }
-}
-
-__global__ void k_poolhead(const float* __restrict__ h, const int* __restrict__ batch,
-                           const float* __restrict__ partIn, const float* __restrict__ gmv,
-                           const float* __restrict__ btv,
-                           const float* __restrict__ fc1w, const float* __restrict__ fc1b,
-                           const float* __restrict__ fc2w, const float* __restrict__ fc2b,
-                           float* __restrict__ out, int n) {
-    __shared__ float tmp[256];
+    if (POOL) {
+        int gm = gmaxs;
+        for (int i = tid; i < (gm + 1) * DOUT; i += 256) {
+            double v = pool_l[i];
+            if (v != 0.) atomicAdd(&pooled[(size_t)gbase * DOUT + i], v);
+        }
+    }
+}
+
+__global__ void __launch_bounds__(128) k_poolhead(
+        const double* __restrict__ pooled, const int* __restrict__ batch,
+        const double* __restrict__ partIn, const float* __restrict__ gmv,
+        const float* __restrict__ btv,
+        const float* __restrict__ fc1w, const float* __restrict__ fc1b,
+        const float* __restrict__ fc2w, const float* __restrict__ fc2b,
+        float* __restrict__ out, int n) {
     __shared__ float pl[128];
     __shared__ float scs[128], shs[128];
     int g = blockIdx.x;
     int tid = threadIdx.x;
-    if (tid < 128) {
-        float s = 0.f, q = 0.f;
-#pragma unroll
-        for (int b2 = 0; b2 < NBUCKET; ++b2) {
-            s += partIn[b2 * 256 + tid];
-            q += partIn[b2 * 256 + 128 + tid];
-        }
-        float mu = s / (float)n;
-        float var = q / (float)n - mu * mu;
-        float a = gmv[tid] * rsqrtf(var + 1e-5f);
-        scs[tid] = a;
-        shs[tid] = btv[tid] - mu * a;
-    }
-    int j = tid & 127, prt = tid >> 7;
+    bn_coef(partIn, gmv, btv, tid, n, scs, shs);
     int a = 0, b = n;
     while (a < b) { int mid = (a + b) >> 1; if (batch[mid] < g) a = mid + 1; else b = mid; }
     int lo = a;
     b = n;
     while (a < b) { int mid = (a + b) >> 1; if (batch[mid] < g + 1) a = mid + 1; else b = mid; }
     int hi = a;
-
-    float acc = 0.f;
-    for (int node = lo + prt; node < hi; node += 2) acc += h[(long)node * 128 + j];
-    tmp[tid] = acc;
-    __syncthreads();
-    if (tid < 128) {
-        float cnt = (float)(hi - lo);
-        float p = scs[tid] * (tmp[tid] + tmp[tid + 128]) + shs[tid] * cnt;
-        pl[tid] = fmaxf(p, 0.f);
-    }
+    float cntf = (float)(hi - lo);
+    float p = scs[tid] * (float)pooled[g * 128 + tid] + shs[tid] * cntf;
+    pl[tid] = fmaxf(p, 0.f);
     __syncthreads();
     if (tid < 64) {
         float v1 = fc1b[tid];
@@ -776,45 +719,49 @@
     int*   bb     = (int*)wsb;    wsb += sizeof(int) * ABLK * NBKT;
     int*   totals = (int*)wsb;    wsb += sizeof(int) * (NBKT + 1);
     wsb = (char*)(((uintptr_t)wsb + 15) & ~(uintptr_t)15);
+    double* part   = (double*)wsb;  wsb += sizeof(double) * 5 * PARTSZ;
+    double* pooled = (double*)wsb;  wsb += sizeof(double) * NG * 128;
     int2*  staging= (int2*)wsb;   wsb += sizeof(int2) * NE;
-    unsigned int* csru = (unsigned int*)wsb; wsb += sizeof(unsigned int) * NE;
-    wsb = (char*)(((uintptr_t)wsb + 15) & ~(uintptr_t)15);
-    float* part   = (float*)wsb;  wsb += sizeof(float) * 5 * PARTSZ;
-    unsigned short* bufB1 = (unsigned short*)wsb;  wsb += sizeof(unsigned short) * (size_t)NN * 64;
-    unsigned short* bufB2 = (unsigned short*)wsb;  wsb += sizeof(unsigned short) * (size_t)NN * 64;
+    int2*  csr    = (int2*)wsb;   wsb += sizeof(int2) * NE;
+    float* bufB1  = (float*)wsb;  wsb += sizeof(float) * (size_t)NN * 64;
+    float* bufB2  = (float*)wsb;  wsb += sizeof(float) * (size_t)NN * 64;
     float* buf1   = (float*)wsb;  wsb += sizeof(float) * (size_t)NN * 64;
-    float* buf2   = (float*)wsb;  wsb += sizeof(float) * (size_t)NN * 128;
+    float* buf2   = (float*)wsb;  wsb += sizeof(float) * (size_t)NN * 16;
 
     const int* row = ei;
     const int* col = ei + NE;
     const int B = 256;
     const int NBF = (NN + 15) / 16;
     const int GB1 = (NN + 127) / 128;
-
-    kA1<<<ABLK, B, 0, stream>>>(col, bb, part, NE);
+    const int ZN = 5 * PARTSZ + NG * 128;
+
+    kA1<<<ABLK, B, 0, stream>>>(col, bb, part, ZN, NE);
     kA2a<<<NBKT, B, 0, stream>>>(bb, totals);
     kA3g<<<ABLK + GB1, B, 0, stream>>>(row, col, ew, bb, totals, staging, x, W[0], buf1, NE, NN);
-    kB<<<NBKT, B, 0, stream>>>(totals, staging, csru, ptr, dis, NN);
-
-    k_l1gather<<<(NN * 4 + 255) / 256, B, 0, stream>>>(buf1, ptr, csru, dis,
+    kB<<<NBKT, B, 0, stream>>>(totals, staging, csr, ptr, dis, NN);
+
+    k_l1gather<<<(NN * 4 + 255) / 256, B, 0, stream>>>(buf1, ptr, csr, dis,
                                                        b[0], part + 0 * PARTSZ, buf2, NN);
 
-    k_fused<16, 32, 4, 1, 0, 1, 0, 1, 16><<<NBF, B, 0, stream>>>(
-        buf2, ptr, csru, dis, part + 0 * PARTSZ, gm[0], bt[0],
+    k_fused<16, 32, 4, 1, 1, 16><<<NBF, B, 0, stream>>>(
+        buf2, ptr, csr, dis, part + 0 * PARTSZ, gm[0], bt[0],
         W[1], b[1], part + 1 * PARTSZ, bufB1, NN);
 
-    k_wgather<32, 1, 0><<<(int)(((long)NN * 16 + 255) / 256), B, 0, stream>>>(
-        bufB1, ptr, csru, dis, part + 1 * PARTSZ, gm[1], bt[1], buf1, NN);
-    k_sgemm<32, 64, 1, 1><<<(NN + 63) / 64, B, 0, stream>>>(buf1, W[2], b[2], part + 2 * PARTSZ, bufB2, NN);
-
-    k_wgather<64, 1, 0><<<(int)(((long)NN * 32 + 255) / 256), B, 0, stream>>>(
-        bufB2, ptr, csru, dis, part + 2 * PARTSZ, gm[2], bt[2], buf1, NN);
-    k_sgemm<64, 64, 0, 1><<<(NN + 63) / 64, B, 0, stream>>>(buf1, W[3], b[3], part + 3 * PARTSZ, bufB1, NN);
-
-    k_wgather<64, 0, 1><<<(int)(((long)NN * 32 + 255) / 256), B, 0, stream>>>(
-        bufB1, ptr, csru, dis, part + 3 * PARTSZ, gm[3], bt[3], buf1, NN);
-    k_sgemm<64, 128, 0, 0><<<(NN + 31) / 32, B, 0, stream>>>(buf1, W[4], b[4], part + 4 * PARTSZ, buf2, NN);
-
-    k_poolhead<<<NG, B, 0, stream>>>(buf2, batch, part + 4 * PARTSZ, gm[4], bt[4],
-                                     fc1w, fc1b, fc2w, fc2b, out, NN);
-}
+    k_wgather<32, 1, 0><<<(int)(((long)NN * 32 + 255) / 256), B, 0, stream>>>(
+        bufB1, ptr, csr, dis, part + 1 * PARTSZ, gm[1], bt[1], buf1, NN);
+    k_sgemm<32, 64, 1, 0><<<(NN + 63) / 64, B, 0, stream>>>(
+        buf1, W[2], b[2], part + 2 * PARTSZ, bufB2, nullptr, nullptr, NN);
+
+    k_wgather<64, 1, 0><<<(int)(((long)NN * 64 + 255) / 256), B, 0, stream>>>(
+        bufB2, ptr, csr, dis, part + 2 * PARTSZ, gm[2], bt[2], buf1, NN);
+    k_sgemm<64, 64, 0, 0><<<(NN + 63) / 64, B, 0, stream>>>(
+        buf1, W[3], b[3], part + 3 * PARTSZ, bufB1, nullptr, nullptr, NN);
+
+    k_wgather<64, 0, 1><<<(int)(((long)NN * 64 + 255) / 256), B, 0, stream>>>(
+        bufB1, ptr, csr, dis, part + 3 * PARTSZ, gm[3], bt[3], buf1, NN);
+    k_sgemm<64, 128, 0, 1><<<(NN + 31) / 32, B, 0, stream>>>(
+        buf1, W[4], b[4], part + 4 * PARTSZ, nullptr, batch, pooled, NN);
+
+    k_poolhead<<<NG, 128, 0, stream>>>(pooled, batch, part + 4 * PARTSZ, gm[4], bt[4],
+                                       fc1w, fc1b, fc2w, fc2b, out, NN);
+}
```

Result: slower. 382.6 us (+5.8%).
